# Kernel optimization log

Hardware: AMD Instinct MI355X
Metric: run time of the kernel (lower is better)

Reference implementation:

```python
import jax, jax.numpy as jnp
import numpy as np

B, S, D = 4, 2048, 1024
E, TOP_K = 8, 2
N_FF = 4096
H = int(2 * N_FF / 3)  # 2730, Expert hidden when ffn_multiplier is None


def setup_inputs() -> dict:
    key = jax.random.key(0)
    ks = jax.random.split(key, 8)
    s = 0.02
    return {
        "x": jax.random.normal(ks[0], (B, S, D), jnp.float32),
        "noise": jax.random.normal(ks[1], (B, S, E), jnp.float32),
        "w_route": jax.random.normal(ks[2], (D, E), jnp.float32) * s,
        "b_route": jnp.zeros((E,), jnp.float32),
        "w_noise": jax.random.normal(ks[3], (D, E), jnp.float32) * s,
        "b_noise": jnp.zeros((E,), jnp.float32),
        "w_proj": jax.random.normal(ks[4], (E, D, 2 * H), jnp.float32) * s,  # SwiGLU proj per expert
        "w_down": jax.random.normal(ks[5], (E, H, D), jnp.float32) * s,
    }


def reference(x, noise, w_route, b_route, w_noise, b_noise, w_proj, w_down):
    b, s, d = x.shape
    e = w_route.shape[1]
    n = b * s
    capacity = int(n * TOP_K / e * 1.0)  # capacity_factor = 1.0

    # --- NoisyTopkRouter (temperature = 1.0) ---
    logits = jnp.einsum("bsd,de->bse", x, w_route) + b_route
    noise_scale = jax.nn.softplus(jnp.einsum("bsd,de->bse", x, w_noise) + b_noise)
    noisy = logits + noise * noise_scale
    top_v, top_i = jax.lax.top_k(noisy, TOP_K)  # [b,s,k]
    # softmax over -inf-filled sparse logits == softmax over the top-k values,
    # scattered back to the expert axis
    probs_k = jax.nn.softmax(top_v, axis=-1)  # [b,s,k]
    routing = jnp.sum(jax.nn.one_hot(top_i, e, dtype=x.dtype) * probs_k[..., None], axis=-2)  # [b,s,e]
    router_prob = routing.mean(axis=(0, 1))
    aux_loss = jnp.sum((router_prob - 1.0 / e) ** 2)

    # --- dispatch ---
    flat_x = x.reshape(n, d)
    flat_gate = routing.reshape(n, e)
    hit = jnp.any(top_i.reshape(n, TOP_K)[:, :, None] == jnp.arange(e)[None, None, :], axis=1)  # [n,e]

    def per_expert(mask_e, gate_e, wp, wd):
        # keep first `capacity` selected tokens, in token order (matches torch nonzero order)
        keep = mask_e & (jnp.cumsum(mask_e) <= capacity)
        sel = jnp.argsort(~keep, stable=True)[:capacity]  # selected token ids first, in order
        valid = keep[sel].astype(flat_x.dtype)
        xin = flat_x[sel]  # [capacity, d]
        x1, x2 = jnp.split(xin @ wp, 2, axis=-1)
        out = (jax.nn.silu(x1) * x2) @ wd  # [capacity, d]
        w = gate_e[sel] * valid
        return sel, out * w[:, None]

    sel, contrib = jax.vmap(per_expert)(hit.T, flat_gate.T, w_proj, w_down)  # [e,cap], [e,cap,d]
    updates = jnp.zeros_like(flat_x).at[sel.reshape(-1)].add(contrib.reshape(-1, d))
    return updates.reshape(b, s, d), aux_loss
```

## Files before the change

### kernel.cpp

```cpp
#include <hip/hip_runtime.h>
#include <cstdint>
#include <cstddef>

#define NTOK 8192
#define DMODEL 1024
#define NEXP 8
#define CAP 2048
#define HFF 2730
#define HFF2 5460
#define KPAD 2752

typedef float f32x4 __attribute__((ext_vector_type(4)));
typedef __attribute__((ext_vector_type(8))) short short8;

__device__ inline unsigned short f2bf(float f) {
  union { float f; unsigned u; } v; v.f = f;
  unsigned u = v.u;
  return (unsigned short)((u + 0x7FFFu + ((u >> 16) & 1u)) >> 16);
}
__device__ inline float bf2f(unsigned short s) {
  union { unsigned u; float f; } v; v.u = ((unsigned)s) << 16; return v.f;
}

typedef __attribute__((address_space(1))) const void g_void;
typedef __attribute__((address_space(3))) void l_void;
__device__ __forceinline__ void dma16(const void* g, void* l) {
  __builtin_amdgcn_global_load_lds((g_void*)g, (l_void*)l, 16, 0, 0);
}

__global__ void cast_x_kernel(const float* __restrict__ x, unsigned short* __restrict__ xb) {
  size_t i = ((size_t)blockIdx.x * 256 + threadIdx.x) * 8;
  float4 v0 = *(const float4*)(x + i);
  float4 v1 = *(const float4*)(x + i + 4);
  union { short8 v; unsigned short s[8]; } p;
  p.s[0] = f2bf(v0.x); p.s[1] = f2bf(v0.y); p.s[2] = f2bf(v0.z); p.s[3] = f2bf(v0.w);
  p.s[4] = f2bf(v1.x); p.s[5] = f2bf(v1.y); p.s[6] = f2bf(v1.z); p.s[7] = f2bf(v1.w);
  *(short8*)(xb + i) = p.v;
}

__global__ void router_kernel(const float* __restrict__ x,
                              const float* __restrict__ noise,
                              const float* __restrict__ w_route,
                              const float* __restrict__ b_route,
                              const float* __restrict__ w_noise,
                              const float* __restrict__ b_noise,
                              int* __restrict__ topi,
                              float* __restrict__ gates) {
  const int lane = threadIdx.x & 63;
  const int wave = threadIdx.x >> 6;
  const int tok = blockIdx.x * 4 + wave;
  const float* xr = x + (size_t)tok * DMODEL;

  double aR[8], aN[8];
#pragma unroll
  for (int e = 0; e < 8; e++) { aR[e] = 0.0; aN[e] = 0.0; }

  for (int d = lane; d < DMODEL; d += 64) {
    double xv = (double)xr[d];
    const float* wr = w_route + d * 8;
    const float* wn = w_noise + d * 8;
#pragma unroll
    for (int e = 0; e < 8; e++) {
      aR[e] += xv * (double)wr[e];
      aN[e] += xv * (double)wn[e];
    }
  }
#pragma unroll
  for (int off = 32; off > 0; off >>= 1) {
#pragma unroll
    for (int e = 0; e < 8; e++) {
      aR[e] += __shfl_down(aR[e], (unsigned)off, 64);
      aN[e] += __shfl_down(aN[e], (unsigned)off, 64);
    }
  }
  if (lane == 0) {
    double nv[8];
#pragma unroll
    for (int e = 0; e < 8; e++) {
      double lg = aR[e] + (double)b_route[e];
      double ns = aN[e] + (double)b_noise[e];
      double sp = fmax(ns, 0.0) + log1p(exp(-fabs(ns)));
      nv[e] = lg + (double)noise[(size_t)tok * 8 + e] * sp;
    }
    int i0 = 0;
#pragma unroll
    for (int e = 1; e < 8; e++) if (nv[e] > nv[i0]) i0 = e;
    int i1 = (i0 == 0) ? 1 : 0;
#pragma unroll
    for (int e = 0; e < 8; e++) if (e != i0 && nv[e] > nv[i1]) i1 = e;
    double r = exp(nv[i1] - nv[i0]);
    float g0 = (float)(1.0 / (1.0 + r));
    float g1 = (float)(r / (1.0 + r));
    topi[tok * 2] = i0; topi[tok * 2 + 1] = i1;
    gates[tok * 2] = g0; gates[tok * 2 + 1] = g1;
  }
}

__global__ void aux_kernel(const int* __restrict__ topi,
                           const float* __restrict__ gates,
                           float* __restrict__ out) {
  const int t = threadIdx.x;
  float s[8];
#pragma unroll
  for (int e = 0; e < 8; e++) s[e] = 0.f;
  for (int i = t; i < NTOK; i += 256) {
    int i0 = topi[2 * i], i1 = topi[2 * i + 1];
    float g0 = gates[2 * i], g1 = gates[2 * i + 1];
#pragma unroll
    for (int e = 0; e < 8; e++)
      s[e] += (i0 == e ? g0 : 0.f) + (i1 == e ? g1 : 0.f);
  }
  __shared__ float sh[256][8];
#pragma unroll
  for (int e = 0; e < 8; e++) sh[t][e] = s[e];
  __syncthreads();
  for (int stride = 128; stride > 0; stride >>= 1) {
    if (t < stride) {
#pragma unroll
      for (int e = 0; e < 8; e++) sh[t][e] += sh[t + stride][e];
    }
    __syncthreads();
  }
  if (t == 0) {
    float aux = 0.f;
#pragma unroll
    for (int e = 0; e < 8; e++) {
      float p = sh[0][e] / (float)NTOK - 0.125f;
      aux += p * p;
    }
    out[(size_t)NTOK * DMODEL] = aux;
  }
}

__global__ void dispatch_kernel(const int* __restrict__ topi,
                                const float* __restrict__ gates,
                                int* __restrict__ sel,
                                float* __restrict__ gsel,
                                int* __restrict__ slot) {
  const int e = blockIdx.x;
  const int t = threadIdx.x;
  const int lane = t & 63;
  const int w = t >> 6;
  __shared__ int waveCnt[16];
  __shared__ int runningS;
  if (t == 0) runningS = 0;
  __syncthreads();

  for (int base = 0; base < NTOK; base += 1024) {
    int tok = base + t;
    int i0 = topi[2 * tok], i1 = topi[2 * tok + 1];
    bool hit = (i0 == e) || (i1 == e);
    int kth = (i0 == e) ? 0 : 1;
    float g = gates[2 * tok + kth];
    unsigned long long m = __ballot(hit);
    int prefix = __popcll(m & ((1ull << lane) - 1ull));
    if (lane == 63) waveCnt[w] = prefix + (hit ? 1 : 0);
    __syncthreads();
    int off = runningS;
    for (int ww = 0; ww < w; ww++) off += waveCnt[ww];
    int pos = off + prefix;
    if (hit) {
      if (pos < CAP) {
        sel[e * CAP + pos] = tok; gsel[e * CAP + pos] = g;
        slot[2 * tok + kth] = pos;
      } else {
        slot[2 * tok + kth] = -1;
      }
    }
    __syncthreads();
    if (t == 0) {
      int sacc = 0;
#pragma unroll
      for (int ww = 0; ww < 16; ww++) sacc += waveCnt[ww];
      runningS += sacc;
    }
    __syncthreads();
  }
  for (int p = runningS + t; p < CAP; p += 1024) { sel[e * CAP + p] = 0; gsel[e * CAP + p] = 0.f; }
}

__global__ void transpose_wp_kernel(const float* __restrict__ wp,
                                    unsigned short* __restrict__ wpT) {
  const int e = blockIdx.z, d0 = blockIdx.y * 64, f0 = blockIdx.x * 64;
  __shared__ unsigned short tile[64][68];
  const int t = threadIdx.x;
  const int ld = t >> 4;
  const int lf4 = (t & 15) * 4;
#pragma unroll
  for (int p = 0; p < 4; p++) {
    int d = d0 + p * 16 + ld;
    int f = f0 + lf4;
    if (f < HFF2) {
      float4 v = *(const float4*)(wp + ((size_t)e * DMODEL + d) * HFF2 + f);
      tile[lf4 + 0][p * 16 + ld] = f2bf(v.x);
      tile[lf4 + 1][p * 16 + ld] = f2bf(v.y);
      tile[lf4 + 2][p * 16 + ld] = f2bf(v.z);
      tile[lf4 + 3][p * 16 + ld] = f2bf(v.w);
    }
  }
  __syncthreads();
  const int dq = (t & 7) * 8;
#pragma unroll
  for (int q = 0; q < 2; q++) {
    int fl = q * 32 + (t >> 3);
    int f = f0 + fl;
    if (f < HFF2) {
      ushort4 u0 = *(const ushort4*)&tile[fl][dq];
      ushort4 u1 = *(const ushort4*)&tile[fl][dq + 4];
      union { ushort4 u[2]; short8 v; } pk;
      pk.u[0] = u0; pk.u[1] = u1;
      *(short8*)(wpT + (size_t)e * HFF2 * DMODEL + (size_t)f * DMODEL + d0 + dq) = pk.v;
    }
  }
}

__global__ void transpose_wd_kernel(const float* __restrict__ wd,
                                    unsigned short* __restrict__ wdT) {
  const int e = blockIdx.z, d0 = blockIdx.y * 32, k0 = blockIdx.x * 32;
  __shared__ unsigned short tile[32][33];
  const int t = threadIdx.x;
  {
    int lk = t >> 3, ld4 = (t & 7) * 4;
    int k = k0 + lk;
    if (k < HFF) {
      float4 v = *(const float4*)(wd + (size_t)e * HFF * DMODEL + (size_t)k * DMODEL + d0 + ld4);
      tile[lk][ld4 + 0] = f2bf(v.x);
      tile[lk][ld4 + 1] = f2bf(v.y);
      tile[lk][ld4 + 2] = f2bf(v.z);
      tile[lk][ld4 + 3] = f2bf(v.w);
    } else {
      tile[lk][ld4 + 0] = 0; tile[lk][ld4 + 1] = 0;
      tile[lk][ld4 + 2] = 0; tile[lk][ld4 + 3] = 0;
    }
  }
  __syncthreads();
  {
    int ld = t >> 3, lkq = (t & 7) * 4;
    ushort4 o = make_ushort4(tile[lkq + 0][ld], tile[lkq + 1][ld],
                             tile[lkq + 2][ld], tile[lkq + 3][ld]);
    *(ushort4*)(wdT + (size_t)e * DMODEL * KPAD + (size_t)(d0 + ld) * KPAD + k0 + lkq) = o;
  }
}

__global__ __launch_bounds__(256, 1)
void gemm1_kernel(const unsigned short* __restrict__ xb,
                  const unsigned short* __restrict__ wpT,
                  const int* __restrict__ sel,
                  unsigned short* __restrict__ h) {
  const int e = blockIdx.z;
  const int m0 = blockIdx.x * 512;
  const int n0 = blockIdx.y * 64;

  __shared__ __align__(16) unsigned short smem[65536];

  const int t = threadIdx.x;
  const int lane = t & 63;
  const int w = t >> 6;
  const int fr = lane & 15;
  const int fq = lane >> 4;
  const int lr = lane >> 2;
  const int lk = (lane & 3) * 8;

  const unsigned short* aSrc[8];
#pragma unroll
  for (int i = 0; i < 8; i++) {
    int tok = sel[e * CAP + m0 + w * 128 + i * 16 + lr];
    aSrc[i] = xb + (size_t)tok * DMODEL + lk;
  }
  const unsigned short* bSrc1[4];
  const unsigned short* bSrc2[4];
#pragma unroll
  for (int j = 0; j < 4; j++) {
    int c = n0 + j * 16 + lr; if (c >= HFF) c = HFF - 1;
    bSrc1[j] = wpT + ((size_t)e * HFF2 + c) * DMODEL + lk;
    bSrc2[j] = wpT + ((size_t)e * HFF2 + HFF + c) * DMODEL + lk;
  }
  char* myLds = (char*)smem + w * 32768;

  auto stage = [&](int kt) {
    char* buf = myLds + (kt & 1) * 16384;
    const int k0 = kt * 32;
#pragma unroll
    for (int i = 0; i < 8; i++) dma16(aSrc[i] + k0, buf + i * 1024);
#pragma unroll
    for (int j = 0; j < 4; j++) {
      dma16(bSrc1[j] + k0, buf + 8192 + j * 1024);
      dma16(bSrc2[j] + k0, buf + 12288 + j * 1024);
    }
  };

  f32x4 acc1[8][4], acc2[8][4];
#pragma unroll
  for (int i = 0; i < 8; i++)
#pragma unroll
    for (int j = 0; j < 4; j++) { acc1[i][j] = (f32x4)0.f; acc2[i][j] = (f32x4)0.f; }

  stage(0); stage(1);

  for (int kt = 0; kt < 32; ++kt) {
    if (kt < 31) asm volatile("s_waitcnt vmcnt(16)" ::: "memory");
    else         asm volatile("s_waitcnt vmcnt(0)" ::: "memory");
    asm volatile("" ::: "memory");

    const char* buf = (const char*)myLds + (kt & 1) * 16384;
    short8 a[8], b1[4], b2[4];
#pragma unroll
    for (int i = 0; i < 8; i++)
      a[i] = *(const short8*)(buf + i * 1024 + fr * 64 + fq * 16);
#pragma unroll
    for (int j = 0; j < 4; j++) {
      b1[j] = *(const short8*)(buf + 8192 + j * 1024 + fr * 64 + fq * 16);
      b2[j] = *(const short8*)(buf + 12288 + j * 1024 + fr * 64 + fq * 16);
    }
    asm volatile("s_waitcnt lgkmcnt(0)" ::: "memory");
    if (kt < 30) stage(kt + 2);
#pragma unroll
    for (int i = 0; i < 8; i++)
#pragma unroll
      for (int j = 0; j < 4; j++) {
        acc1[i][j] = __builtin_amdgcn_mfma_f32_16x16x32_bf16(a[i], b1[j], acc1[i][j], 0, 0, 0);
        acc2[i][j] = __builtin_amdgcn_mfma_f32_16x16x32_bf16(a[i], b2[j], acc2[i][j], 0, 0, 0);
      }
  }

#pragma unroll
  for (int i = 0; i < 8; i++) {
#pragma unroll
    for (int j = 0; j < 4; j++) {
      const int col = n0 + j * 16 + fr;
#pragma unroll
      for (int r = 0; r < 4; r++) {
        const int row = m0 + w * 128 + i * 16 + fq * 4 + r;
        float v1 = acc1[i][j][r], v2 = acc2[i][j][r];
        float hv = (col < HFF) ? (v1 / (1.f + __expf(-v1))) * v2 : 0.f;
        h[((size_t)e * CAP + row) * KPAD + col] = f2bf(hv);
      }
    }
  }
}

__global__ __launch_bounds__(256, 1)
void gemm2_kernel(const unsigned short* __restrict__ h,
                  const unsigned short* __restrict__ wdT,
                  unsigned short* __restrict__ contrib) {
  const int e = blockIdx.z;
  const int m0 = blockIdx.x * 512;
  const int n0 = blockIdx.y * 128;

  __shared__ __align__(16) unsigned short smem[65536];

  const int t = threadIdx.x;
  const int lane = t & 63;
  const int w = t >> 6;
  const int fr = lane & 15;
  const int fq = lane >> 4;
  const int lr = lane >> 2;
  const int lk = (lane & 3) * 8;

  const unsigned short* aSrc[8];
#pragma unroll
  for (int i = 0; i < 8; i++)
    aSrc[i] = h + ((size_t)e * CAP + m0 + w * 128 + i * 16 + lr) * KPAD + lk;
  const unsigned short* bSrc[8];
#pragma unroll
  for (int j = 0; j < 8; j++)
    bSrc[j] = wdT + ((size_t)e * DMODEL + n0 + j * 16 + lr) * KPAD + lk;

  char* myLds = (char*)smem + w * 32768;

  auto stage = [&](int kt) {
    char* buf = myLds + (kt & 1) * 16384;
    const int k0 = kt * 32;
#pragma unroll
    for (int i = 0; i < 8; i++) dma16(aSrc[i] + k0, buf + i * 1024);
#pragma unroll
    for (int j = 0; j < 8; j++) dma16(bSrc[j] + k0, buf + 8192 + j * 1024);
  };

  f32x4 acc[8][8];
#pragma unroll
  for (int i = 0; i < 8; i++)
#pragma unroll
    for (int j = 0; j < 8; j++) acc[i][j] = (f32x4)0.f;

  stage(0); stage(1);

  for (int kt = 0; kt < 86; ++kt) {
    if (kt < 85) asm volatile("s_waitcnt vmcnt(16)" ::: "memory");
    else         asm volatile("s_waitcnt vmcnt(0)" ::: "memory");
    asm volatile("" ::: "memory");

    const char* buf = (const char*)myLds + (kt & 1) * 16384;
    short8 a[8], b[8];
#pragma unroll
    for (int i = 0; i < 8; i++)
      a[i] = *(const short8*)(buf + i * 1024 + fr * 64 + fq * 16);
#pragma unroll
    for (int j = 0; j < 8; j++)
      b[j] = *(const short8*)(buf + 8192 + j * 1024 + fr * 64 + fq * 16);
    asm volatile("s_waitcnt lgkmcnt(0)" ::: "memory");
    if (kt < 84) stage(kt + 2);
#pragma unroll
    for (int i = 0; i < 8; i++)
#pragma unroll
      for (int j = 0; j < 8; j++)
        acc[i][j] = __builtin_amdgcn_mfma_f32_16x16x32_bf16(a[i], b[j], acc[i][j], 0, 0, 0);
  }

#pragma unroll
  for (int i = 0; i < 8; i++) {
#pragma unroll
    for (int j = 0; j < 8; j++) {
      const int col = n0 + j * 16 + fr;
#pragma unroll
      for (int r = 0; r < 4; r++) {
        const int row = m0 + w * 128 + i * 16 + fq * 4 + r;
        contrib[((size_t)e * CAP + row) * DMODEL + col] = f2bf(acc[i][j][r]);
      }
    }
  }
}

__global__ void combine_kernel(const unsigned short* __restrict__ contrib,
                               const int* __restrict__ topi,
                               const int* __restrict__ slot,
                               const float* __restrict__ gates,
                               float* __restrict__ out) {
  const int tok = blockIdx.x;
  const int t = threadIdx.x;
  const int e0 = topi[2 * tok], e1 = topi[2 * tok + 1];
  const int s0 = slot[2 * tok], s1 = slot[2 * tok + 1];
  const float g0 = gates[2 * tok], g1 = gates[2 * tok + 1];
  float4 acc = make_float4(0.f, 0.f, 0.f, 0.f);
  if (s0 >= 0) {
    ushort4 c = *(const ushort4*)(contrib + ((size_t)(e0 * CAP + s0)) * DMODEL + t * 4);
    acc.x += g0 * bf2f(c.x); acc.y += g0 * bf2f(c.y);
    acc.z += g0 * bf2f(c.z); acc.w += g0 * bf2f(c.w);
  }
  if (s1 >= 0) {
    ushort4 c = *(const ushort4*)(contrib + ((size_t)(e1 * CAP + s1)) * DMODEL + t * 4);
    acc.x += g1 * bf2f(c.x); acc.y += g1 * bf2f(c.y);
    acc.z += g1 * bf2f(c.z); acc.w += g1 * bf2f(c.w);
  }
  *(float4*)(out + (size_t)tok * DMODEL + t * 4) = acc;
}

extern "C" void kernel_launch(void* const* d_in, const int* in_sizes, int n_in,
                              void* d_out, int out_size, void* d_ws, size_t ws_size,
                              hipStream_t stream) {
  const float* x = (const float*)d_in[0];
  const float* noise = (const float*)d_in[1];
  const float* w_route = (const float*)d_in[2];
  const float* b_route = (const float*)d_in[3];
  const float* w_noise = (const float*)d_in[4];
  const float* b_noise = (const float*)d_in[5];
  const float* w_proj = (const float*)d_in[6];
  const float* w_down = (const float*)d_in[7];
  float* out = (float*)d_out;

  char* ws = (char*)d_ws;
  const size_t WT_BYTES = (size_t)NEXP * HFF2 * DMODEL * 2;
  const size_t WDT_BYTES = (size_t)NEXP * DMODEL * KPAD * 2;
  const size_t H_BYTES = (size_t)NEXP * CAP * KPAD * 2;
  unsigned short* wT = (unsigned short*)ws;
  unsigned short* contrib = (unsigned short*)(ws + WDT_BYTES);
  unsigned short* hbuf = (unsigned short*)(ws + WT_BYTES);
  char* p = ws + WT_BYTES + H_BYTES;
  int* sel = (int*)p;          p += (size_t)NEXP * CAP * 4;
  float* gsel = (float*)p;     p += (size_t)NEXP * CAP * 4;
  int* topi = (int*)p;         p += (size_t)NTOK * 2 * 4;
  float* gates = (float*)p;    p += (size_t)NTOK * 2 * 4;
  int* slot = (int*)p;

  unsigned short* xb = (unsigned short*)d_out;

  hipLaunchKernelGGL(cast_x_kernel, dim3(NTOK * DMODEL / (256 * 8)), dim3(256), 0, stream, x, xb);
  hipLaunchKernelGGL(router_kernel, dim3(NTOK / 4), dim3(256), 0, stream,
                     x, noise, w_route, b_route, w_noise, b_noise, topi, gates);
  hipLaunchKernelGGL(dispatch_kernel, dim3(NEXP), dim3(1024), 0, stream, topi, gates, sel, gsel, slot);
  hipLaunchKernelGGL(transpose_wp_kernel, dim3(86, 16, NEXP), dim3(256), 0, stream, w_proj, wT);
  hipLaunchKernelGGL(gemm1_kernel, dim3(CAP / 512, KPAD / 64, NEXP), dim3(256), 0, stream,
                     xb, wT, sel, hbuf);
  hipLaunchKernelGGL(transpose_wd_kernel, dim3(KPAD / 32, DMODEL / 32, NEXP), dim3(256), 0, stream, w_down, wT);
  hipLaunchKernelGGL(gemm2_kernel, dim3(CAP / 512, DMODEL / 128, NEXP), dim3(256), 0, stream,
                     hbuf, wT, contrib);
  hipLaunchKernelGGL(combine_kernel, dim3(NTOK), dim3(256), 0, stream,
                     contrib, topi, slot, gates, out);
  hipLaunchKernelGGL(aux_kernel, dim3(1), dim3(256), 0, stream, topi, gates, out);
}
```

Measured before the change: 847.1 us.

## Load GEMM A operand directly to registers, swizzle B in LDS, allow two blocks/CU

In both expert GEMMs the A operand (gathered tokens or hidden activations) is now loaded straight from global memory into registers in MFMA fragment layout, double-buffered across k-steps. Only the weight operand still goes through LDS. Halving the LDS footprint lets launch_bounds request two blocks per CU. An XOR swizzle on the B tile layout is meant to avoid LDS bank conflicts. The risks are that the direct global loads are only 16-byte row fragments, which may coalesce poorly, and that the extra register buffers may spill under the tighter two-block register budget, since the accumulators already use many VGPRs.

```diff
diff --git a/kernel.cpp b/kernel.cpp
--- a/kernel.cpp
+++ b/kernel.cpp
@@ -242,7 +242,7 @@
   }
 }
 
-__global__ __launch_bounds__(256, 1)
+__global__ __launch_bounds__(256, 2)
 void gemm1_kernel(const unsigned short* __restrict__ xb,
                   const unsigned short* __restrict__ wpT,
                   const int* __restrict__ sel,
@@ -251,7 +251,7 @@
   const int m0 = blockIdx.x * 512;
   const int n0 = blockIdx.y * 64;
 
-  __shared__ __align__(16) unsigned short smem[65536];
+  __shared__ __align__(16) unsigned short smem[32768];
 
   const int t = threadIdx.x;
   const int lane = t & 63;
@@ -259,33 +259,33 @@
   const int fr = lane & 15;
   const int fq = lane >> 4;
   const int lr = lane >> 2;
-  const int lk = (lane & 3) * 8;
+  const int lks = ((lane & 3) ^ ((lane >> 3) & 3)) * 8;
+  const int rb = fr * 64 + (fq ^ ((fr >> 1) & 3)) * 16;
 
   const unsigned short* aSrc[8];
 #pragma unroll
   for (int i = 0; i < 8; i++) {
-    int tok = sel[e * CAP + m0 + w * 128 + i * 16 + lr];
-    aSrc[i] = xb + (size_t)tok * DMODEL + lk;
+    int tok = sel[e * CAP + m0 + w * 128 + i * 16 + fr];
+    aSrc[i] = xb + (size_t)tok * DMODEL + fq * 8;
   }
   const unsigned short* bSrc1[4];
   const unsigned short* bSrc2[4];
 #pragma unroll
   for (int j = 0; j < 4; j++) {
     int c = n0 + j * 16 + lr; if (c >= HFF) c = HFF - 1;
-    bSrc1[j] = wpT + ((size_t)e * HFF2 + c) * DMODEL + lk;
-    bSrc2[j] = wpT + ((size_t)e * HFF2 + HFF + c) * DMODEL + lk;
-  }
-  char* myLds = (char*)smem + w * 32768;
-
-  auto stage = [&](int kt) {
-    char* buf = myLds + (kt & 1) * 16384;
+    bSrc1[j] = wpT + ((size_t)e * HFF2 + c) * DMODEL + lks;
+    bSrc2[j] = wpT + ((size_t)e * HFF2 + HFF + c) * DMODEL + lks;
+  }
+
+  char* myLds = (char*)smem + w * 16384;
+
+  auto stageB = [&](int kt) {
+    char* buf = myLds + (kt & 1) * 8192;
     const int k0 = kt * 32;
 #pragma unroll
-    for (int i = 0; i < 8; i++) dma16(aSrc[i] + k0, buf + i * 1024);
-#pragma unroll
     for (int j = 0; j < 4; j++) {
-      dma16(bSrc1[j] + k0, buf + 8192 + j * 1024);
-      dma16(bSrc2[j] + k0, buf + 12288 + j * 1024);
+      dma16(bSrc1[j] + k0, buf + j * 1024);
+      dma16(bSrc2[j] + k0, buf + 4096 + j * 1024);
     }
   };
 
@@ -295,33 +295,38 @@
 #pragma unroll
     for (int j = 0; j < 4; j++) { acc1[i][j] = (f32x4)0.f; acc2[i][j] = (f32x4)0.f; }
 
-  stage(0); stage(1);
-
-  for (int kt = 0; kt < 32; ++kt) {
-    if (kt < 31) asm volatile("s_waitcnt vmcnt(16)" ::: "memory");
-    else         asm volatile("s_waitcnt vmcnt(0)" ::: "memory");
-    asm volatile("" ::: "memory");
-
-    const char* buf = (const char*)myLds + (kt & 1) * 16384;
-    short8 a[8], b1[4], b2[4];
+  short8 aA[8], aB[8];
+  stageB(0);
+#pragma unroll
+  for (int i = 0; i < 8; i++) aA[i] = *(const short8*)(aSrc[i]);
+  stageB(1);
+
+  auto step = [&](int kt, short8 (&aC)[8], short8 (&aN)[8]) {
+    asm volatile("s_waitcnt vmcnt(16)" ::: "memory");
+    const char* buf = (const char*)myLds + (kt & 1) * 8192;
+    short8 b1[4], b2[4];
+#pragma unroll
+    for (int j = 0; j < 4; j++) {
+      b1[j] = *(const short8*)(buf + j * 1024 + rb);
+      b2[j] = *(const short8*)(buf + 4096 + j * 1024 + rb);
+    }
+    asm volatile("s_waitcnt lgkmcnt(0)" ::: "memory");
+    if (kt < 30) stageB(kt + 2);
+    if (kt < 31) {
+      const int k1 = (kt + 1) * 32;
+#pragma unroll
+      for (int i = 0; i < 8; i++) aN[i] = *(const short8*)(aSrc[i] + k1);
+    }
 #pragma unroll
     for (int i = 0; i < 8; i++)
-      a[i] = *(const short8*)(buf + i * 1024 + fr * 64 + fq * 16);
-#pragma unroll
-    for (int j = 0; j < 4; j++) {
-      b1[j] = *(const short8*)(buf + 8192 + j * 1024 + fr * 64 + fq * 16);
-      b2[j] = *(const short8*)(buf + 12288 + j * 1024 + fr * 64 + fq * 16);
-    }
-    asm volatile("s_waitcnt lgkmcnt(0)" ::: "memory");
-    if (kt < 30) stage(kt + 2);
-#pragma unroll
-    for (int i = 0; i < 8; i++)
 #pragma unroll
       for (int j = 0; j < 4; j++) {
-        acc1[i][j] = __builtin_amdgcn_mfma_f32_16x16x32_bf16(a[i], b1[j], acc1[i][j], 0, 0, 0);
-        acc2[i][j] = __builtin_amdgcn_mfma_f32_16x16x32_bf16(a[i], b2[j], acc2[i][j], 0, 0, 0);
+        acc1[i][j] = __builtin_amdgcn_mfma_f32_16x16x32_bf16(aC[i], b1[j], acc1[i][j], 0, 0, 0);
+        acc2[i][j] = __builtin_amdgcn_mfma_f32_16x16x32_bf16(aC[i], b2[j], acc2[i][j], 0, 0, 0);
       }
-  }
+  };
+
+  for (int kt = 0; kt < 32; kt += 2) { step(kt, aA, aB); step(kt + 1, aB, aA); }
 
 #pragma unroll
   for (int i = 0; i < 8; i++) {
@@ -347,7 +352,7 @@
   const int m0 = blockIdx.x * 512;
   const int n0 = blockIdx.y * 128;
 
-  __shared__ __align__(16) unsigned short smem[65536];
+  __shared__ __align__(16) unsigned short smem[32768];
 
   const int t = threadIdx.x;
   const int lane = t & 63;
@@ -355,26 +360,23 @@
   const int fr = lane & 15;
   const int fq = lane >> 4;
   const int lr = lane >> 2;
-  const int lk = (lane & 3) * 8;
+  const int lks = ((lane & 3) ^ ((lane >> 3) & 3)) * 8;
+  const int rb = fr * 64 + (fq ^ ((fr >> 1) & 3)) * 16;
 
   const unsigned short* aSrc[8];
 #pragma unroll
   for (int i = 0; i < 8; i++)
-    aSrc[i] = h + ((size_t)e * CAP + m0 + w * 128 + i * 16 + lr) * KPAD + lk;
-  const unsigned short* bSrc[8];
-#pragma unroll
-  for (int j = 0; j < 8; j++)
-    bSrc[j] = wdT + ((size_t)e * DMODEL + n0 + j * 16 + lr) * KPAD + lk;
-
-  char* myLds = (char*)smem + w * 32768;
-
-  auto stage = [&](int kt) {
-    char* buf = myLds + (kt & 1) * 16384;
+    aSrc[i] = h + ((size_t)e * CAP + m0 + w * 128 + i * 16 + fr) * KPAD + fq * 8;
+  const unsigned short* bBase = wdT + ((size_t)e * DMODEL + n0 + lr) * KPAD + lks;
+
+  char* myLds = (char*)smem + w * 16384;
+
+  auto stageB = [&](int kt) {
+    char* buf = myLds + (kt & 1) * 8192;
     const int k0 = kt * 32;
 #pragma unroll
-    for (int i = 0; i < 8; i++) dma16(aSrc[i] + k0, buf + i * 1024);
-#pragma unroll
-    for (int j = 0; j < 8; j++) dma16(bSrc[j] + k0, buf + 8192 + j * 1024);
+    for (int j = 0; j < 8; j++)
+      dma16(bBase + (size_t)j * 16 * KPAD + k0, buf + j * 1024);
   };
 
   f32x4 acc[8][8];
@@ -383,29 +385,34 @@
 #pragma unroll
     for (int j = 0; j < 8; j++) acc[i][j] = (f32x4)0.f;
 
-  stage(0); stage(1);
-
-  for (int kt = 0; kt < 86; ++kt) {
-    if (kt < 85) asm volatile("s_waitcnt vmcnt(16)" ::: "memory");
-    else         asm volatile("s_waitcnt vmcnt(0)" ::: "memory");
-    asm volatile("" ::: "memory");
-
-    const char* buf = (const char*)myLds + (kt & 1) * 16384;
-    short8 a[8], b[8];
+  short8 aA[8], aB[8];
+  stageB(0);
+#pragma unroll
+  for (int i = 0; i < 8; i++) aA[i] = *(const short8*)(aSrc[i]);
+  stageB(1);
+
+  auto step = [&](int kt, short8 (&aC)[8], short8 (&aN)[8]) {
+    asm volatile("s_waitcnt vmcnt(16)" ::: "memory");
+    const char* buf = (const char*)myLds + (kt & 1) * 8192;
+    short8 b[8];
+#pragma unroll
+    for (int j = 0; j < 8; j++)
+      b[j] = *(const short8*)(buf + j * 1024 + rb);
+    asm volatile("s_waitcnt lgkmcnt(0)" ::: "memory");
+    if (kt < 84) stageB(kt + 2);
+    if (kt < 85) {
+      const int k1 = (kt + 1) * 32;
+#pragma unroll
+      for (int i = 0; i < 8; i++) aN[i] = *(const short8*)(aSrc[i] + k1);
+    }
 #pragma unroll
     for (int i = 0; i < 8; i++)
-      a[i] = *(const short8*)(buf + i * 1024 + fr * 64 + fq * 16);
-#pragma unroll
-    for (int j = 0; j < 8; j++)
-      b[j] = *(const short8*)(buf + 8192 + j * 1024 + fr * 64 + fq * 16);
-    asm volatile("s_waitcnt lgkmcnt(0)" ::: "memory");
-    if (kt < 84) stage(kt + 2);
-#pragma unroll
-    for (int i = 0; i < 8; i++)
 #pragma unroll
       for (int j = 0; j < 8; j++)
-        acc[i][j] = __builtin_amdgcn_mfma_f32_16x16x32_bf16(a[i], b[j], acc[i][j], 0, 0, 0);
-  }
+        acc[i][j] = __builtin_amdgcn_mfma_f32_16x16x32_bf16(aC[i], b[j], acc[i][j], 0, 0, 0);
+  };
+
+  for (int kt = 0; kt < 86; kt += 2) { step(kt, aA, aB); step(kt + 1, aB, aA); }
 
 #pragma unroll
   for (int i = 0; i < 8; i++) {
```

Measured after the change: 2.485 ms. 193% more time.
